# Kernel tuning notes

Hardware: AMD Instinct MI355X
Metric: run time of the kernel (lower is better)

The kernel has to match this reference:

```python
import jax, jax.numpy as jnp
import numpy as np

D_MODEL = 1024
N_HEADS = 16
HEAD_DIM = D_MODEL // N_HEADS


def setup_inputs() -> dict:
    key = jax.random.key(0)
    k_x, k_wqkv, k_bqkv, k_wo, k_bo = jax.random.split(key, 5)
    B, T = 2, 2048
    scale = 1.0 / np.sqrt(D_MODEL)
    return {
        "x": jax.random.normal(k_x, (B, T, D_MODEL), dtype=jnp.float32),
        "W_qkv": jax.random.normal(k_wqkv, (D_MODEL, 3 * D_MODEL), dtype=jnp.float32) * scale,
        "b_qkv": jax.random.normal(k_bqkv, (3 * D_MODEL,), dtype=jnp.float32) * 0.01,
        "W_out": jax.random.normal(k_wo, (D_MODEL, D_MODEL), dtype=jnp.float32) * scale,
        "b_out": jax.random.normal(k_bo, (D_MODEL,), dtype=jnp.float32) * 0.01,
    }


def reference(x, W_qkv, b_qkv, W_out, b_out):
    B, T, C = x.shape
    qkv = x @ W_qkv + b_qkv                      # [B,T,3C]
    q, k, v = jnp.split(qkv, 3, axis=-1)
    def heads(t):
        return t.reshape(B, T, N_HEADS, HEAD_DIM).transpose(0, 2, 1, 3)  # [B,H,T,d]
    q, k, v = heads(q), heads(k), heads(v)
    att = jnp.einsum('bhqd,bhkd->bhqk', q, k) / np.sqrt(HEAD_DIM)
    causal = jnp.tril(jnp.ones((T, T), dtype=bool))
    att = jnp.where(causal, att, -jnp.inf)
    att = jax.nn.softmax(att, axis=-1)
    out = jnp.einsum('bhqk,bhkd->bhqd', att, v)  # [B,H,T,d]
    out = out.transpose(0, 2, 1, 3).reshape(B, T, C)
    return out @ W_out + b_out
```

## Files before the change

kernel.cpp:

```cpp
#include <hip/hip_runtime.h>
#include <hip/hip_bf16.h>
#include <math.h>

typedef __bf16 bf16;
typedef __attribute__((ext_vector_type(8))) __bf16 bf16x8;
typedef __attribute__((ext_vector_type(4))) __bf16 bf16x4;
typedef __attribute__((ext_vector_type(4))) short s16x4;
typedef __attribute__((ext_vector_type(4))) float f32x4;
typedef __attribute__((ext_vector_type(16))) float f32x16;
typedef __attribute__((ext_vector_type(4))) unsigned u32x4;

#define T_SEQ 2048

static __device__ __forceinline__ float fast_exp2(float x) {
#if __has_builtin(__builtin_amdgcn_exp2f)
    return __builtin_amdgcn_exp2f(x);
#else
    return __expf(x * 0.69314718f);
#endif
}

static __device__ __forceinline__ unsigned pk(float lo, float hi) {
    unsigned a = (unsigned)__builtin_bit_cast(unsigned short, (bf16)lo);
    unsigned b = (unsigned)__builtin_bit_cast(unsigned short, (bf16)hi);
    return a | (b << 16);
}

static __device__ __forceinline__ void gload_lds16(const bf16* g, bf16* l) {
    __builtin_amdgcn_global_load_lds((const __attribute__((address_space(1))) void*)g,
                                     (__attribute__((address_space(3))) void*)l, 16, 0, 0);
}

static __device__ __forceinline__ int swz(int row, int colb) {
    return row * 128 + (colb ^ ((row & 7) << 4));
}

__global__ void convert_kernel(const float* __restrict__ x, bf16* __restrict__ xb, int n4)
{
    int i = blockIdx.x * blockDim.x + threadIdx.x;
    int stride = gridDim.x * blockDim.x;
    for (; i < n4; i += stride) {
        f32x4 v = ((const f32x4*)x)[i];
        bf16x4 o;
        o[0] = (bf16)v[0]; o[1] = (bf16)v[1]; o[2] = (bf16)v[2]; o[3] = (bf16)v[3];
        ((bf16x4*)xb)[i] = o;
    }
}

__global__ __launch_bounds__(256) void transpose_conv_kernel(
    const float* __restrict__ W, bf16* __restrict__ Wt, int K, int N)
{
    __shared__ float tile[32][33];
    int tx = threadIdx.x & 31, ty = threadIdx.x >> 5;
    int n0 = blockIdx.x * 32, k0 = blockIdx.y * 32;
#pragma unroll
    for (int j = 0; j < 4; ++j)
        tile[ty + j * 8][tx] = W[(size_t)(k0 + ty + j * 8) * N + n0 + tx];
    __syncthreads();
#pragma unroll
    for (int j = 0; j < 4; ++j)
        Wt[(size_t)(n0 + ty + j * 8) * K + k0 + tx] = (bf16)tile[tx][ty + j * 8];
}

__global__ __launch_bounds__(256) void vtrans_kernel(
    const bf16* __restrict__ qkv, bf16* __restrict__ Vt)
{
    __shared__ bf16 tile[64][72];
    const int tid = threadIdx.x;
    const int bh = blockIdx.y, b = bh >> 4, h = bh & 15;
    const int t0 = blockIdx.x * 64;
    const size_t base = (size_t)b * T_SEQ * 3072 + 2048 + h * 64;
    const int r = tid >> 3, c = (tid & 7) * 8;
    *(bf16x8*)&tile[r][c]      = *(const bf16x8*)&qkv[base + (size_t)(t0 + r) * 3072 + c];
    *(bf16x8*)&tile[r + 32][c] = *(const bf16x8*)&qkv[base + (size_t)(t0 + r + 32) * 3072 + c];
    __syncthreads();
    bf16x8 o0, o1;
#pragma unroll
    for (int j = 0; j < 8; ++j) { o0[j] = tile[c + j][r]; o1[j] = tile[c + j][r + 32]; }
    *(bf16x8*)&Vt[((size_t)bh * 64 + r) * T_SEQ + t0 + c] = o0;
    *(bf16x8*)&Vt[((size_t)bh * 64 + r + 32) * T_SEQ + t0 + c] = o1;
}

template<int BM, int BN, int BLK, int WGN, int OUT_BF16>
__global__ __launch_bounds__(BLK, 2) void gemm2ph_kernel(
    const bf16* __restrict__ A, const bf16* __restrict__ Bt,
    const float* __restrict__ bias, void* __restrict__ Cout,
    int M, int N, int K, int GX)
{
    constexpr int WAVES = BLK / 64, WGM = WAVES / WGN;
    constexpr int MR = BM / (WGM * 16), NR = BN / (WGN * 16);
    constexpr int A_RND = BM * 8 / BLK, B_RND = BN * 8 / BLK;
    constexpr int LDS_HALF = (BM + BN) * 128;
    __shared__ __align__(16) char lds[2 * LDS_HALF];

    const int tid = threadIdx.x, lane = tid & 63, wid = tid >> 6;
    const int wm = wid / WGN, wn = wid % WGN;
    const int l15 = lane & 15, l4 = lane >> 4;
    const int cpx = gridDim.x >> 3;
    const int sbid = ((int)blockIdx.x & 7) * cpx + ((int)blockIdx.x >> 3);
    const int m0 = (sbid / GX) * BM, n0 = (sbid % GX) * BN;
    const int wu = tid & ~63;

    f32x4 acc[MR][NR] = {};
    const int NT = K >> 6;

    auto stage = [&](int b, int kt) {
        char* Ab = lds + b * LDS_HALF;
        char* Bb = Ab + BM * 128;
#pragma unroll
        for (int j = 0; j < A_RND; ++j) {
            int ch = j * BLK + tid, r = ch >> 3;
            int c = ((ch & 7) ^ (r & 7)) * 8;
            gload_lds16(&A[(size_t)(m0 + r) * K + kt + c],
                        (bf16*)Ab + (size_t)(j * BLK + wu) * 8);
        }
#pragma unroll
        for (int j = 0; j < B_RND; ++j) {
            int ch = j * BLK + tid, r = ch >> 3;
            int c = ((ch & 7) ^ (r & 7)) * 8;
            gload_lds16(&Bt[(size_t)(n0 + r) * K + kt + c],
                        (bf16*)Bb + (size_t)(j * BLK + wu) * 8);
        }
    };

    stage(0, 0);
    asm volatile("s_waitcnt vmcnt(0)" ::: "memory");
    __builtin_amdgcn_s_barrier();

    for (int t = 0; t < NT; ++t) {
        if (t + 1 < NT) stage((t + 1) & 1, (t + 1) * 64);
        const char* Ab = lds + (t & 1) * LDS_HALF;
        const char* Bb = Ab + BM * 128;
#pragma unroll
        for (int kk = 0; kk < 2; ++kk) {
            bf16x8 af[MR], bfr[NR];
#pragma unroll
            for (int mi = 0; mi < MR; ++mi) {
                int row = wm * (MR * 16) + mi * 16 + l15;
                af[mi] = *(const bf16x8*)(Ab + swz(row, kk * 64 + l4 * 16));
            }
#pragma unroll
            for (int ni = 0; ni < NR; ++ni) {
                int row = wn * (NR * 16) + ni * 16 + l15;
                bfr[ni] = *(const bf16x8*)(Bb + swz(row, kk * 64 + l4 * 16));
            }
#pragma unroll
            for (int mi = 0; mi < MR; ++mi)
#pragma unroll
                for (int ni = 0; ni < NR; ++ni)
                    acc[mi][ni] = __builtin_amdgcn_mfma_f32_16x16x32_bf16(
                        af[mi], bfr[ni], acc[mi][ni], 0, 0, 0);
        }
        asm volatile("s_waitcnt vmcnt(0)" ::: "memory");
        __builtin_amdgcn_s_barrier();
    }

#pragma unroll
    for (int mi = 0; mi < MR; ++mi) {
#pragma unroll
        for (int ni = 0; ni < NR; ++ni) {
            int col = n0 + wn * (NR * 16) + ni * 16 + l15;
            float bv = bias[col];
#pragma unroll
            for (int r = 0; r < 4; ++r) {
                int row = m0 + wm * (MR * 16) + mi * 16 + l4 * 4 + r;
                float v = acc[mi][ni][r] + bv;
                if (OUT_BF16) ((bf16*)Cout)[(size_t)row * N + col] = (bf16)v;
                else          ((float*)Cout)[(size_t)row * N + col] = v;
            }
        }
    }
}

__global__ __launch_bounds__(256, 3) void attn_kernel(
    const bf16* __restrict__ qkv, const bf16* __restrict__ Vt, bf16* __restrict__ attb)
{
    __shared__ __align__(16) char smem[32768];
    const int tid = threadIdx.x, lane = tid & 63, wid = tid >> 6;
    const int qg = wid >> 1, par = wid & 1;
    const int bid = blockIdx.x;
    const int iq = 31 - (bid >> 5);
    const int bh = bid & 31, b = bh >> 4, h = bh & 15;
    const int nt = iq + 1, npairs = (nt + 1) >> 1;
    const int l31 = lane & 31, hi = lane >> 5, hib = hi * 16;
    const size_t base = (size_t)b * T_SEQ * 3072;
    const int koff = 1024 + h * 64;
    const size_t vtb = (size_t)bh * 64 * T_SEQ;
    const int sr = tid >> 2, sq4 = tid & 3;

    const int q0 = iq * 64 + qg * 32;
    const int qrow = q0 + l31;

    bf16x8 Qf[4];
#pragma unroll
    for (int ds = 0; ds < 4; ++ds)
        Qf[ds] = *(const bf16x8*)&qkv[base + (size_t)qrow * 3072 + h * 64 + ds * 16 + hi * 8];

    f32x16 Oacc[2] = {};
    float m_run = -1e30f, l_run = 0.f;

    bf16x8 kreg[2][2], vreg[2][2];
    {
#pragma unroll
        for (int p = 0; p < 2; ++p)
#pragma unroll
            for (int j = 0; j < 2; ++j) {
                kreg[p][j] = *(const bf16x8*)&qkv[base + (size_t)(p * 64 + sr) * 3072
                                                 + koff + sq4 * 16 + j * 8];
                vreg[p][j] = *(const bf16x8*)&Vt[vtb + (size_t)sr * T_SEQ + p * 64 + sq4 * 16 + j * 8];
            }
    }

    for (int u = 0; u < npairs; ++u) {
        __syncthreads();
#pragma unroll
        for (int p = 0; p < 2; ++p) {
            char* Kp = smem + p * 8192;
            char* Vp = smem + 16384 + p * 8192;
#pragma unroll
            for (int j = 0; j < 2; ++j) {
                const int byte = swz(sr, sq4 * 32 + j * 16);
                *(bf16x8*)(Kp + byte) = kreg[p][j];
                *(bf16x8*)(Vp + byte) = vreg[p][j];
            }
        }
        __syncthreads();
        if (u + 1 < npairs) {
            const int pb = (u + 1) * 128;
#pragma unroll
            for (int p = 0; p < 2; ++p)
#pragma unroll
                for (int j = 0; j < 2; ++j) {
                    kreg[p][j] = *(const bf16x8*)&qkv[base + (size_t)(pb + p * 64 + sr) * 3072
                                                     + koff + sq4 * 16 + j * 8];
                    vreg[p][j] = *(const bf16x8*)&Vt[vtb + (size_t)sr * T_SEQ + pb + p * 64 + sq4 * 16 + j * 8];
                }
        }
        const int t = 2 * u + par;
        if (t < nt) {
            const char* Kc = smem + par * 8192;
            const char* Vc = smem + 16384 + par * 8192;
            f32x16 S[2] = {};
            __builtin_amdgcn_s_setprio(1);
#pragma unroll
            for (int ds = 0; ds < 4; ++ds)
#pragma unroll
                for (int kt = 0; kt < 2; ++kt) {
                    bf16x8 af = *(const bf16x8*)(Kc + swz(kt * 32 + l31, ds * 32 + hib));
                    S[kt] = __builtin_amdgcn_mfma_f32_32x32x16_bf16(af, Qf[ds], S[kt], 0, 0, 0);
                }
            __builtin_amdgcn_s_setprio(0);
            float pmax = -3.0e38f;
            if (t == nt - 1) {
                const int qloc = qg * 32 + l31;
#pragma unroll
                for (int kt = 0; kt < 2; ++kt)
#pragma unroll
                    for (int j = 0; j < 16; ++j) {
                        const int kloc = kt * 32 + (j & 3) + 8 * (j >> 2) + 4 * hi;
                        if (kloc > qloc) S[kt][j] = -3.0e38f;
                        pmax = fmaxf(pmax, S[kt][j]);
                    }
            } else {
#pragma unroll
                for (int kt = 0; kt < 2; ++kt)
#pragma unroll
                    for (int j = 0; j < 16; ++j) pmax = fmaxf(pmax, S[kt][j]);
            }
            pmax = fmaxf(pmax, __shfl_xor(pmax, 32));
            if (!__all(pmax - m_run <= 64.f)) {
                float mnew = fmaxf(m_run, pmax);
                float alpha = fast_exp2((m_run - mnew) * 0.18033688f);
                m_run = mnew;
                l_run *= alpha;
                Oacc[0] *= alpha;
                Oacc[1] *= alpha;
            }
            float lsum = 0.f;
#pragma unroll
            for (int kt = 0; kt < 2; ++kt)
#pragma unroll
                for (int j = 0; j < 16; ++j) {
                    float p = fast_exp2((S[kt][j] - m_run) * 0.18033688f);
                    S[kt][j] = p;
                    lsum += p;
                }
            lsum += __shfl_xor(lsum, 32);
            l_run += lsum;
            __builtin_amdgcn_s_setprio(1);
#pragma unroll
            for (int ks = 0; ks < 4; ++ks) {
                const int kt = ks >> 1, bs = (ks & 1) * 8;
                unsigned P01 = pk(S[kt][bs + 0], S[kt][bs + 1]);
                unsigned P23 = pk(S[kt][bs + 2], S[kt][bs + 3]);
                unsigned P45 = pk(S[kt][bs + 4], S[kt][bs + 5]);
                unsigned P67 = pk(S[kt][bs + 6], S[kt][bs + 7]);
                auto r02 = __builtin_amdgcn_permlane32_swap(P01, P45, false, false);
                auto r13 = __builtin_amdgcn_permlane32_swap(P23, P67, false, false);
                u32x4 wv;
                wv[0] = r02[0]; wv[1] = r13[0]; wv[2] = r02[1]; wv[3] = r13[1];
                bf16x8 Bfrag = __builtin_bit_cast(bf16x8, wv);
#pragma unroll
                for (int dt = 0; dt < 2; ++dt) {
                    bf16x8 av = *(const bf16x8*)(Vc + swz(dt * 32 + l31, ks * 32 + hib));
                    Oacc[dt] = __builtin_amdgcn_mfma_f32_32x32x16_bf16(av, Bfrag, Oacc[dt], 0, 0, 0);
                }
            }
            __builtin_amdgcn_s_setprio(0);
        }
    }

    float* cbuf = (float*)smem;
    __syncthreads();
    if (par == 1) {
        float* p = cbuf + (qg * 64 + lane) * 36;
#pragma unroll
        for (int dt = 0; dt < 2; ++dt)
#pragma unroll
            for (int j = 0; j < 16; ++j) p[dt * 16 + j] = Oacc[dt][j];
        p[32] = m_run; p[33] = l_run;
    }
    __syncthreads();
    if (par == 0) {
        const float* p = cbuf + (qg * 64 + lane) * 36;
        float m1 = p[32], l1 = p[33];
        float m = fmaxf(m_run, m1);
        float a0 = fast_exp2((m_run - m) * 0.18033688f);
        float a1 = fast_exp2((m1 - m) * 0.18033688f);
        float inv = 1.f / (l_run * a0 + l1 * a1);
#pragma unroll
        for (int dt = 0; dt < 2; ++dt) {
#pragma unroll
            for (int g = 0; g < 4; ++g) {
                bf16x4 o;
#pragma unroll
                for (int j = 0; j < 4; ++j)
                    o[j] = (bf16)((Oacc[dt][g * 4 + j] * a0 + p[dt * 16 + g * 4 + j] * a1) * inv);
                const int d = dt * 32 + g * 8 + 4 * hi;
                *(bf16x4*)&attb[((size_t)b * T_SEQ + qrow) * 1024 + h * 64 + d] = o;
            }
        }
    }
}

extern "C" void kernel_launch(void* const* d_in, const int* in_sizes, int n_in,
                              void* d_out, int out_size, void* d_ws, size_t ws_size,
                              hipStream_t stream)
{
    const float* x    = (const float*)d_in[0];
    const float* Wqkv = (const float*)d_in[1];
    const float* bqkv = (const float*)d_in[2];
    const float* Wout = (const float*)d_in[3];
    const float* bout = (const float*)d_in[4];
    float* out = (float*)d_out;

    char* ws = (char*)d_ws;
    bf16* xb    = (bf16*)(ws);
    bf16* Vt    = (bf16*)(ws);
    bf16* Wqkvt = (bf16*)(ws + (8ull  << 20));
    bf16* Woutt = (bf16*)(ws + (14ull << 20));
    bf16* qkvb  = (bf16*)(ws + (16ull << 20));
    bf16* attb  = (bf16*)(ws + (40ull << 20));

    convert_kernel<<<dim3(2048), dim3(256), 0, stream>>>(x, xb, (4096 * 1024) / 4);
    transpose_conv_kernel<<<dim3(96, 32), dim3(256), 0, stream>>>(Wqkv, Wqkvt, 1024, 3072);
    transpose_conv_kernel<<<dim3(32, 32), dim3(256), 0, stream>>>(Wout, Woutt, 1024, 1024);
    gemm2ph_kernel<256, 192, 512, 4, 1><<<dim3(256), dim3(512), 0, stream>>>(
        xb, Wqkvt, bqkv, (void*)qkvb, 4096, 3072, 1024, 16);
    vtrans_kernel<<<dim3(32, 32), dim3(256), 0, stream>>>(qkvb, Vt);
    attn_kernel<<<dim3(1024), dim3(256), 0, stream>>>(qkvb, Vt, attb);
    gemm2ph_kernel<128, 128, 256, 2, 0><<<dim3(256), dim3(256), 0, stream>>>(
        attb, Woutt, bout, (void*)out, 4096, 1024, 1024, 8);
}
```

Measured before the change: 101.5 us.

## Compute softmax row sums via MFMA with ones and retile QKV GEMM

The attention kernel drops the per-element scalar row-sum accumulation and its cross-lane shuffle. Instead it accumulates the softmax denominator with an extra MFMA that multiplies the bf16 probabilities by a matrix of ones. The exponent's subtract-and-scale is folded into a single FMA, and the max reduction is reordered. Separately, the QKV GEMM launch moves to smaller tiles with more blocks. The changes trade VALU work for one extra MFMA per k-step and use bf16-rounded probabilities in the denominator.

```diff
diff --git a/kernel.cpp b/kernel.cpp
--- a/kernel.cpp
+++ b/kernel.cpp
@@ -5,7 +5,6 @@
 typedef __bf16 bf16;
 typedef __attribute__((ext_vector_type(8))) __bf16 bf16x8;
 typedef __attribute__((ext_vector_type(4))) __bf16 bf16x4;
-typedef __attribute__((ext_vector_type(4))) short s16x4;
 typedef __attribute__((ext_vector_type(4))) float f32x4;
 typedef __attribute__((ext_vector_type(16))) float f32x16;
 typedef __attribute__((ext_vector_type(4))) unsigned u32x4;
@@ -196,8 +195,13 @@
     for (int ds = 0; ds < 4; ++ds)
         Qf[ds] = *(const bf16x8*)&qkv[base + (size_t)qrow * 3072 + h * 64 + ds * 16 + hi * 8];
 
+    bf16x8 onesA;
+#pragma unroll
+    for (int j = 0; j < 8; ++j) onesA[j] = (bf16)1.0f;
+
     f32x16 Oacc[2] = {};
-    float m_run = -1e30f, l_run = 0.f;
+    f32x16 lacc = {};
+    float m_run = -1e30f;
 
     bf16x8 kreg[2][2], vreg[2][2];
     {
@@ -250,7 +254,6 @@
                     S[kt] = __builtin_amdgcn_mfma_f32_32x32x16_bf16(af, Qf[ds], S[kt], 0, 0, 0);
                 }
             __builtin_amdgcn_s_setprio(0);
-            float pmax = -3.0e38f;
             if (t == nt - 1) {
                 const int qloc = qg * 32 + l31;
 #pragma unroll
@@ -259,34 +262,29 @@
                     for (int j = 0; j < 16; ++j) {
                         const int kloc = kt * 32 + (j & 3) + 8 * (j >> 2) + 4 * hi;
                         if (kloc > qloc) S[kt][j] = -3.0e38f;
-                        pmax = fmaxf(pmax, S[kt][j]);
                     }
-            } else {
-#pragma unroll
-                for (int kt = 0; kt < 2; ++kt)
-#pragma unroll
-                    for (int j = 0; j < 16; ++j) pmax = fmaxf(pmax, S[kt][j]);
-            }
+            }
+            float pmax = -3.0e38f;
+#pragma unroll
+            for (int kt = 0; kt < 2; ++kt)
+#pragma unroll
+                for (int j = 0; j < 16; j += 2)
+                    pmax = fmaxf(fmaxf(S[kt][j], S[kt][j + 1]), pmax);
             pmax = fmaxf(pmax, __shfl_xor(pmax, 32));
             if (!__all(pmax - m_run <= 64.f)) {
                 float mnew = fmaxf(m_run, pmax);
                 float alpha = fast_exp2((m_run - mnew) * 0.18033688f);
                 m_run = mnew;
-                l_run *= alpha;
                 Oacc[0] *= alpha;
                 Oacc[1] *= alpha;
-            }
-            float lsum = 0.f;
+                lacc *= alpha;
+            }
+            const float mc = m_run * 0.18033688f;
 #pragma unroll
             for (int kt = 0; kt < 2; ++kt)
 #pragma unroll
-                for (int j = 0; j < 16; ++j) {
-                    float p = fast_exp2((S[kt][j] - m_run) * 0.18033688f);
-                    S[kt][j] = p;
-                    lsum += p;
-                }
-            lsum += __shfl_xor(lsum, 32);
-            l_run += lsum;
+                for (int j = 0; j < 16; ++j)
+                    S[kt][j] = fast_exp2(__builtin_fmaf(S[kt][j], 0.18033688f, -mc));
             __builtin_amdgcn_s_setprio(1);
 #pragma unroll
             for (int ks = 0; ks < 4; ++ks) {
@@ -305,6 +303,7 @@
                     bf16x8 av = *(const bf16x8*)(Vc + swz(dt * 32 + l31, ks * 32 + hib));
                     Oacc[dt] = __builtin_amdgcn_mfma_f32_32x32x16_bf16(av, Bfrag, Oacc[dt], 0, 0, 0);
                 }
+                lacc = __builtin_amdgcn_mfma_f32_32x32x16_bf16(onesA, Bfrag, lacc, 0, 0, 0);
             }
             __builtin_amdgcn_s_setprio(0);
         }
@@ -318,7 +317,7 @@
         for (int dt = 0; dt < 2; ++dt)
 #pragma unroll
             for (int j = 0; j < 16; ++j) p[dt * 16 + j] = Oacc[dt][j];
-        p[32] = m_run; p[33] = l_run;
+        p[32] = m_run; p[33] = lacc[0];
     }
     __syncthreads();
     if (par == 0) {
@@ -327,7 +326,7 @@
         float m = fmaxf(m_run, m1);
         float a0 = fast_exp2((m_run - m) * 0.18033688f);
         float a1 = fast_exp2((m1 - m) * 0.18033688f);
-        float inv = 1.f / (l_run * a0 + l1 * a1);
+        float inv = 1.f / (lacc[0] * a0 + l1 * a1);
 #pragma unroll
         for (int dt = 0; dt < 2; ++dt) {
 #pragma unroll
@@ -365,7 +364,7 @@
     convert_kernel<<<dim3(2048), dim3(256), 0, stream>>>(x, xb, (4096 * 1024) / 4);
     transpose_conv_kernel<<<dim3(96, 32), dim3(256), 0, stream>>>(Wqkv, Wqkvt, 1024, 3072);
     transpose_conv_kernel<<<dim3(32, 32), dim3(256), 0, stream>>>(Wout, Woutt, 1024, 1024);
-    gemm2ph_kernel<256, 192, 512, 4, 1><<<dim3(256), dim3(512), 0, stream>>>(
+    gemm2ph_kernel<128, 192, 256, 2, 1><<<dim3(512), dim3(256), 0, stream>>>(
         xb, Wqkvt, bqkv, (void*)qkvb, 4096, 3072, 1024, 16);
     vtrans_kernel<<<dim3(32, 32), dim3(256), 0, stream>>>(qkvb, Vt);
     attn_kernel<<<dim3(1024), dim3(256), 0, stream>>>(qkvb, Vt, attb);
```

Result: no change. 100.0 us (-1.5%).
